# Kernel optimization log

Hardware: AMD Instinct MI355X
Metric: run time of the kernel (lower is better)

The kernel has to match this reference:

```python
import jax, jax.numpy as jnp
import numpy as np

B, S, D = 4, 4096, 256

def setup_inputs() -> dict:
    key = jax.random.key(0)
    ks = jax.random.split(key, 7)
    scale = 1.0 / np.sqrt(D)
    return {
        "x": jax.random.normal(ks[0], (B, S, D), dtype=jnp.float32),
        "Wq": jax.random.normal(ks[1], (D, D), dtype=jnp.float32) * scale,
        "bq": jnp.zeros((D,), dtype=jnp.float32),
        "Wk": jax.random.normal(ks[2], (D, D), dtype=jnp.float32) * scale,
        "bk": jnp.zeros((D,), dtype=jnp.float32),
        "Wv": jax.random.normal(ks[3], (D, D), dtype=jnp.float32) * scale,
        "bv": jnp.zeros((D,), dtype=jnp.float32),
    }

def reference(x, Wq, bq, Wk, bk, Wv, bv):
    # Dense projections (Keras Dense: x @ W + b)
    q = x @ Wq + bq  # [B,S,D]
    k = x @ Wk + bk
    v = x @ Wv + bv
    # Unscaled attention: softmax(Q K^T) V + residual
    scores = jnp.einsum("bsd,btd->bst", q, k)  # [B,S,S]
    attn = jax.nn.softmax(scores, axis=-1)
    out = jnp.einsum("bst,btd->bsd", attn, v)
    return out + x
```

## Files before the change

kernel.cpp:

```cpp
#include <hip/hip_runtime.h>
#include <stdint.h>

#define NB   4
#define SEQ  4096
#define DIM  256
#define NROW (NB*SEQ)

using bf16x8   = __attribute__((ext_vector_type(8))) __bf16;
using half8    = __attribute__((ext_vector_type(8))) _Float16;
using f32x4    = __attribute__((ext_vector_type(4))) float;
using f32x16   = __attribute__((ext_vector_type(16))) float;
using u32x4    = __attribute__((ext_vector_type(4))) unsigned int;
using ushort4t = __attribute__((ext_vector_type(4))) unsigned short;

__device__ __forceinline__ unsigned f2bf(float f){
    unsigned u = __builtin_bit_cast(unsigned, f);
    return (u + 0x7fffu + ((u >> 16) & 1u)) >> 16;
}
__device__ __forceinline__ float bf2f(unsigned b){
    return __builtin_bit_cast(float, b << 16);
}

#define MFMA(a,b,c)   __builtin_amdgcn_mfma_f32_16x16x32_bf16((a),(b),(c),0,0,0)
#define MFMAQK(a,b,c) __builtin_amdgcn_mfma_f32_32x32x16_f16((a),(b),(c),0,0,0)
#define MFMAPV(a,b,c) __builtin_amdgcn_mfma_f32_32x32x16_bf16((a),(b),(c),0,0,0)

__device__ __forceinline__ void gld16(const void* g, void* l){
    __builtin_amdgcn_global_load_lds(
        (const __attribute__((address_space(1))) void*)g,
        (__attribute__((address_space(3))) void*)l, 16, 0, 0);
}

__global__ __launch_bounds__(256) void convert_w_kernel(
    const float* __restrict__ Wq, const float* __restrict__ Wk,
    const float* __restrict__ Wv,
    unsigned short* __restrict__ WtHi, unsigned short* __restrict__ WtLo)
{
    int mat = blockIdx.y;
    const float* W = (mat == 0) ? Wq : (mat == 1 ? Wk : Wv);
    int id = blockIdx.x * 256 + threadIdx.x;
    int k = id >> 8, n = id & 255;
    float v = W[id];
    unsigned hi = f2bf(v);
    unsigned lo = f2bf(v - bf2f(hi));
    int nh = n >> 7, nt = (n >> 4) & 7, q16 = n & 15;
    int kc = k >> 5, g = (k >> 3) & 3, j = k & 7;
    int lane = g * 16 + q16;
    int o = ((((mat * 2 + nh) * 8 + nt) * 8 + kc) * 64 + lane) * 8 + j;
    WtHi[o] = (unsigned short)hi;
    WtLo[o] = (unsigned short)lo;
}

__global__ __launch_bounds__(256) void proj_kernel(
    const float* __restrict__ x,
    const unsigned short* __restrict__ WtHi, const unsigned short* __restrict__ WtLo,
    const float* __restrict__ bq, const float* __restrict__ bk,
    const float* __restrict__ bv,
    _Float16* __restrict__ Qf, _Float16* __restrict__ Kf,
    unsigned short* __restrict__ Vt)
{
    const int tid = threadIdx.x, lane = tid & 63, wid = tid >> 6;
    const int g = lane >> 4, q16 = lane & 15;
    const int mbase = blockIdx.x * 64 + wid * 16;
    const int nh = blockIdx.y;

    f32x4 acc[3][8];
    #pragma unroll
    for (int m = 0; m < 3; m++)
        #pragma unroll
        for (int n = 0; n < 8; n++) acc[m][n] = f32x4{0.f, 0.f, 0.f, 0.f};

    const float* xr = x + (mbase + q16) * DIM;

    for (int kc = 0; kc < 8; kc++) {
        const float* p = xr + kc * 32 + 8 * g;
        f32x4 va = *(const f32x4*)p;
        f32x4 vb = *(const f32x4*)(p + 4);
        float fv[8] = {va[0], va[1], va[2], va[3], vb[0], vb[1], vb[2], vb[3]};
        unsigned hw[4], lw[4];
        #pragma unroll
        for (int i = 0; i < 4; i++) {
            unsigned h0 = f2bf(fv[2*i]),              h1 = f2bf(fv[2*i+1]);
            unsigned l0 = f2bf(fv[2*i]   - bf2f(h0)), l1 = f2bf(fv[2*i+1] - bf2f(h1));
            hw[i] = h0 | (h1 << 16);
            lw[i] = l0 | (l1 << 16);
        }
        bf16x8 ahi = __builtin_bit_cast(bf16x8, u32x4{hw[0], hw[1], hw[2], hw[3]});
        bf16x8 alo = __builtin_bit_cast(bf16x8, u32x4{lw[0], lw[1], lw[2], lw[3]});

        #pragma unroll
        for (int mat = 0; mat < 3; mat++) {
            #pragma unroll
            for (int nt = 0; nt < 8; nt++) {
                const int fbase =
                    ((((mat * 2 + nh) * 8 + nt) * 8 + kc) * 64 + lane) * 8;
                bf16x8 bh = *(const bf16x8*)(WtHi + fbase);
                bf16x8 bl = *(const bf16x8*)(WtLo + fbase);
                acc[mat][nt] = MFMA(ahi, bh, acc[mat][nt]);
                acc[mat][nt] = MFMA(ahi, bl, acc[mat][nt]);
                acc[mat][nt] = MFMA(alo, bh, acc[mat][nt]);
            }
        }
    }

    #pragma unroll
    for (int nt = 0; nt < 8; nt++) {
        int ncol = nh * 128 + nt * 16 + q16;
        {
            float bb = bq[ncol];
            f32x4 c = acc[0][nt];
            #pragma unroll
            for (int r = 0; r < 4; r++)
                Qf[(size_t)(mbase + 4*g + r) * DIM + ncol] = (_Float16)(c[r] + bb);
        }
        {
            float bb = bk[ncol];
            f32x4 c = acc[1][nt];
            #pragma unroll
            for (int r = 0; r < 4; r++)
                Kf[(size_t)(mbase + 4*g + r) * DIM + ncol] = (_Float16)(c[r] + bb);
        }
        {
            float bb = bv[ncol];
            f32x4 c = acc[2][nt];
            ushort4t pk;
            #pragma unroll
            for (int r = 0; r < 4; r++) pk[r] = (unsigned short)f2bf(c[r] + bb);
            int m0 = mbase + 4 * g;
            int bat = m0 >> 12, s0 = m0 & 4095;
            *(ushort4t*)(Vt + (size_t)(bat * DIM + ncol) * SEQ + s0) = pk;
        }
    }
}

#define KLDS  0
#define VLDS  32768
#define BUFSZ 65536

__global__ __launch_bounds__(512, 1) void flash_kernel(
    const _Float16* __restrict__ Qf, const _Float16* __restrict__ Kf,
    const unsigned short* __restrict__ Vt,
    unsigned short* __restrict__ O0, unsigned short* __restrict__ O1,
    unsigned short* __restrict__ O2, unsigned short* __restrict__ O3,
    float2* __restrict__ ml0, float2* __restrict__ ml1,
    float2* __restrict__ ml2, float2* __restrict__ ml3)
{
    __shared__ __align__(16) unsigned char smem[131072];

    const int tid = threadIdx.x, lane = tid & 63, wid = tid >> 6;
    const int r32 = lane & 31, h = lane >> 5;
    const int qrow0 = blockIdx.x * 256;
    const int b = qrow0 >> 12;
    const int split = blockIdx.y;
    const int kvbase = split * 1024;
    const int stp = wid & 1;

    half8 qf[16];
    {
        const _Float16* qp = Qf + (size_t)(qrow0 + wid * 32 + r32) * DIM;
        #pragma unroll
        for (int s = 0; s < 16; s++)
            qf[s] = *(const half8*)(qp + s * 16 + h * 8);
    }

    f32x16 o[8];
    #pragma unroll
    for (int i = 0; i < 8; i++)
        #pragma unroll
        for (int j = 0; j < 16; j++) o[i][j] = 0.f;
    float m_run = -3.0e38f, l_run = 0.f;

    auto stage = [&](int chunk, int buf) {
        const int kv0 = kvbase + chunk * 64;
        unsigned char* base = smem + buf * BUFSZ;
        #pragma unroll
        for (int i = 0; i < 4; i++) {
            const int t = wid * 4 + i;
            const int krow = 2 * t + h;
            const int ksl  = (lane & 31) ^ (krow & 7);
            gld16(Kf + (size_t)(b * SEQ + kv0 + krow) * DIM + ksl * 8,
                  base + KLDS + t * 1024);
            const int d   = 8 * t + (lane >> 3);
            const int vsl = (lane & 7) ^ (d & 7);
            gld16(Vt + (size_t)(b * DIM + d) * SEQ + kv0 + vsl * 8,
                  base + VLDS + t * 1024);
        }
    };

    stage(0, 0);
    __syncthreads();

    for (int c = 0; c < 16; c++) {
        const int bf = c & 1;
        if (c + 1 < 16) stage(c + 1, bf ^ 1);

        const unsigned char* kb = smem + bf * BUFSZ;
        const unsigned char* vb = kb + VLDS;

        #pragma unroll
        for (int ii = 0; ii < 2; ii++) {
            const int st = ii ^ stp;
            f32x16 a;
            #pragma unroll
            for (int j = 0; j < 16; j++) a[j] = 0.f;
            __builtin_amdgcn_s_setprio(1);
            #pragma unroll
            for (int s = 0; s < 16; s++) {
                const int off = (st * 32 + r32) * 512
                              + (((2 * s + h) ^ (r32 & 7)) * 16);
                half8 kf = *(const half8*)(kb + KLDS + off);
                a = MFMAQK(kf, qf[s], a);
            }
            __builtin_amdgcn_s_setprio(0);

            float pm = a[0];
            #pragma unroll
            for (int j = 1; j < 16; j++) pm = fmaxf(pm, a[j]);
            pm = fmaxf(pm, __shfl_xor(pm, 32, 64));
            const bool defer = __all(pm <= m_run + 8.0f) != 0;
            const float mn = defer ? m_run : fmaxf(m_run, pm);
            const float sc = defer ? 1.0f : __expf(m_run - mn);
            float e[16]; float ps = 0.f;
            #pragma unroll
            for (int j = 0; j < 16; j++) { e[j] = __expf(a[j] - mn); ps += e[j]; }
            ps += __shfl_xor(ps, 32, 64);
            l_run = l_run * sc + ps;
            m_run = mn;

            unsigned w[8];
            #pragma unroll
            for (int t = 0; t < 8; t++)
                asm("v_cvt_pk_bf16_f32 %0, %1, %2"
                    : "=v"(w[t]) : "v"(e[2 * t]), "v"(e[2 * t + 1]));
            asm volatile("v_permlane32_swap_b32 %0, %1" : "+v"(w[0]), "+v"(w[2]));
            asm volatile("v_permlane32_swap_b32 %0, %1" : "+v"(w[1]), "+v"(w[3]));
            asm volatile("v_permlane32_swap_b32 %0, %1" : "+v"(w[4]), "+v"(w[6]));
            asm volatile("v_permlane32_swap_b32 %0, %1" : "+v"(w[5]), "+v"(w[7]));
            bf16x8 pA = __builtin_bit_cast(bf16x8, u32x4{w[0], w[1], w[2], w[3]});
            bf16x8 pB = __builtin_bit_cast(bf16x8, u32x4{w[4], w[5], w[6], w[7]});

            __builtin_amdgcn_s_setprio(1);
            #pragma unroll
            for (int dt = 0; dt < 8; dt++) {
                const int d = dt * 32 + r32;
                const int sw = d & 7;
                bf16x8 v0 = *(const bf16x8*)(vb + d * 128
                               + (((st * 4 + h)     ^ sw) * 16));
                bf16x8 v1 = *(const bf16x8*)(vb + d * 128
                               + (((st * 4 + 2 + h) ^ sw) * 16));
                f32x16 oo = o[dt];
                if (!defer) {
                    #pragma unroll
                    for (int j = 0; j < 16; j++) oo[j] *= sc;
                }
                oo = MFMAPV(v0, pA, oo);
                oo = MFMAPV(v1, pB, oo);
                o[dt] = oo;
            }
            __builtin_amdgcn_s_setprio(0);
        }

        __syncthreads();
    }

    if (h == 0) {
        float2* mlp = (split == 0) ? ml0 : (split == 1) ? ml1
                    : (split == 2) ? ml2 : ml3;
        mlp[qrow0 + wid * 32 + r32] = float2{m_run, l_run};
    }

    unsigned short* oP = (split == 0) ? O0 : (split == 1) ? O1
                       : (split == 2) ? O2 : O3;
    float* T = (float*)smem;
    #pragma unroll
    for (int dt = 0; dt < 8; dt++) {
        __syncthreads();
        #pragma unroll
        for (int j = 0; j < 16; j++) {
            const int dloc = (j & 3) + 8 * (j >> 2) + 4 * h;
            T[(wid * 32 + r32) * 33 + dloc] = o[dt][j];
        }
        __syncthreads();
        #pragma unroll
        for (int rq = 0; rq < 4; rq++) {
            const int q = wid * 32 + rq * 8 + (lane >> 3);
            const float* tr = T + q * 33 + (lane & 7) * 4;
            ushort4t pk;
            #pragma unroll
            for (int r = 0; r < 4; r++) pk[r] = (unsigned short)f2bf(tr[r]);
            *(ushort4t*)(oP + (size_t)(qrow0 + q) * DIM
                         + dt * 32 + (lane & 7) * 4) = pk;
        }
    }
}

__global__ __launch_bounds__(256) void combine_kernel(
    const unsigned short* __restrict__ o0, const unsigned short* __restrict__ o1,
    const unsigned short* __restrict__ o2, const unsigned short* __restrict__ o3,
    const float2* __restrict__ ml0, const float2* __restrict__ ml1,
    const float2* __restrict__ ml2, const float2* __restrict__ ml3,
    const float* __restrict__ x, float* __restrict__ out)
{
    int row = blockIdx.x * 4 + (threadIdx.x >> 6);
    int c0  = (threadIdx.x & 63) * 4;
    float2 A = ml0[row], B = ml1[row], C = ml2[row], D = ml3[row];
    float M  = fmaxf(fmaxf(A.x, B.x), fmaxf(C.x, D.x));
    float w0 = __expf(A.x - M), w1 = __expf(B.x - M);
    float w2 = __expf(C.x - M), w3 = __expf(D.x - M);
    float inv = 1.0f / (w0 * A.y + w1 * B.y + w2 * C.y + w3 * D.y);
    size_t base = (size_t)row * DIM + c0;
    ushort4t u0 = *(const ushort4t*)(o0 + base);
    ushort4t u1 = *(const ushort4t*)(o1 + base);
    ushort4t u2 = *(const ushort4t*)(o2 + base);
    ushort4t u3 = *(const ushort4t*)(o3 + base);
    f32x4    xr = *(const f32x4*)(x + base);
    f32x4 res;
    #pragma unroll
    for (int j = 0; j < 4; j++)
        res[j] = (w0 * bf2f((unsigned)u0[j]) + w1 * bf2f((unsigned)u1[j])
                + w2 * bf2f((unsigned)u2[j]) + w3 * bf2f((unsigned)u3[j])) * inv
                + xr[j];
    *(f32x4*)(out + base) = res;
}

extern "C" void kernel_launch(void* const* d_in, const int* in_sizes, int n_in,
                              void* d_out, int out_size, void* d_ws, size_t ws_size,
                              hipStream_t stream)
{
    const float* x  = (const float*)d_in[0];
    const float* Wq = (const float*)d_in[1];
    const float* bq = (const float*)d_in[2];
    const float* Wk = (const float*)d_in[3];
    const float* bk = (const float*)d_in[4];
    const float* Wv = (const float*)d_in[5];
    const float* bv = (const float*)d_in[6];
    float* out = (float*)d_out;

    unsigned char* ws = (unsigned char*)d_ws;
    _Float16*       Qf   = (_Float16*)(ws);
    _Float16*       Kf   = (_Float16*)(ws +  8388608);
    unsigned short* Vt   = (unsigned short*)(ws + 16777216);
    unsigned short* WtHi = (unsigned short*)(ws + 25165824);
    unsigned short* WtLo = (unsigned short*)(ws + 25559040);
    unsigned short* O0   = (unsigned short*)(ws + 25952256);
    unsigned short* O1   = (unsigned short*)(ws + 34340864);
    unsigned short* O2   = (unsigned short*)(ws + 42729472);
    unsigned short* O3   = (unsigned short*)(ws + 51118080);
    float2*         ML0  = (float2*)       (ws + 59506688);
    float2*         ML1  = (float2*)       (ws + 59637760);
    float2*         ML2  = (float2*)       (ws + 59768832);
    float2*         ML3  = (float2*)       (ws + 59899904);

    convert_w_kernel<<<dim3(256, 3), 256, 0, stream>>>(Wq, Wk, Wv, WtHi, WtLo);
    proj_kernel<<<dim3(256, 2), 256, 0, stream>>>(x, WtHi, WtLo, bq, bk, bv,
                                                  Qf, Kf, Vt);
    flash_kernel<<<dim3(64, 4), 512, 0, stream>>>(Qf, Kf, Vt,
                                                  O0, O1, O2, O3,
                                                  ML0, ML1, ML2, ML3);
    combine_kernel<<<4096, 256, 0, stream>>>(O0, O1, O2, O3,
                                             ML0, ML1, ML2, ML3, x, out);
}
```

Baseline: 181.1 us.

## Stage projection weights in LDS and split QK MFMA chain into two accumulators

```diff
diff --git a/kernel.cpp b/kernel.cpp
--- a/kernel.cpp
+++ b/kernel.cpp
@@ -59,6 +59,8 @@
     _Float16* __restrict__ Qf, _Float16* __restrict__ Kf,
     unsigned short* __restrict__ Vt)
 {
+    __shared__ __align__(16) unsigned char wsm[49152];
+
     const int tid = threadIdx.x, lane = tid & 63, wid = tid >> 6;
     const int g = lane >> 4, q16 = lane & 15;
     const int mbase = blockIdx.x * 64 + wid * 16;
@@ -73,6 +75,16 @@
     const float* xr = x + (mbase + q16) * DIM;
 
     for (int kc = 0; kc < 8; kc++) {
+        __syncthreads();
+        #pragma unroll
+        for (int i = 0; i < 12; i++) {
+            const int idx = wid * 12 + i;
+            const int mat = idx >> 4, nt = (idx >> 1) & 7, pl = idx & 1;
+            const size_t fb =
+                ((size_t)(((mat * 2 + nh) * 8 + nt) * 8 + kc)) * 512 + lane * 8;
+            gld16((pl ? WtLo : WtHi) + fb, wsm + idx * 1024);
+        }
+
         const float* p = xr + kc * 32 + 8 * g;
         f32x4 va = *(const f32x4*)p;
         f32x4 vb = *(const f32x4*)(p + 4);
@@ -88,14 +100,15 @@
         bf16x8 ahi = __builtin_bit_cast(bf16x8, u32x4{hw[0], hw[1], hw[2], hw[3]});
         bf16x8 alo = __builtin_bit_cast(bf16x8, u32x4{lw[0], lw[1], lw[2], lw[3]});
 
+        __syncthreads();
+
         #pragma unroll
         for (int mat = 0; mat < 3; mat++) {
             #pragma unroll
             for (int nt = 0; nt < 8; nt++) {
-                const int fbase =
-                    ((((mat * 2 + nh) * 8 + nt) * 8 + kc) * 64 + lane) * 8;
-                bf16x8 bh = *(const bf16x8*)(WtHi + fbase);
-                bf16x8 bl = *(const bf16x8*)(WtLo + fbase);
+                const int sidx = mat * 16 + nt * 2;
+                bf16x8 bh = *(const bf16x8*)(wsm + sidx * 1024 + lane * 16);
+                bf16x8 bl = *(const bf16x8*)(wsm + (sidx + 1) * 1024 + lane * 16);
                 acc[mat][nt] = MFMA(ahi, bh, acc[mat][nt]);
                 acc[mat][nt] = MFMA(ahi, bl, acc[mat][nt]);
                 acc[mat][nt] = MFMA(alo, bh, acc[mat][nt]);
@@ -200,18 +213,22 @@
         #pragma unroll
         for (int ii = 0; ii < 2; ii++) {
             const int st = ii ^ stp;
-            f32x16 a;
-            #pragma unroll
-            for (int j = 0; j < 16; j++) a[j] = 0.f;
+            f32x16 a0, a1;
+            #pragma unroll
+            for (int j = 0; j < 16; j++) { a0[j] = 0.f; a1[j] = 0.f; }
             __builtin_amdgcn_s_setprio(1);
             #pragma unroll
-            for (int s = 0; s < 16; s++) {
-                const int off = (st * 32 + r32) * 512
-                              + (((2 * s + h) ^ (r32 & 7)) * 16);
-                half8 kf = *(const half8*)(kb + KLDS + off);
-                a = MFMAQK(kf, qf[s], a);
+            for (int s = 0; s < 16; s += 2) {
+                const int rb = (st * 32 + r32) * 512;
+                const int off0 = rb + (((2 * s + h)     ^ (r32 & 7)) * 16);
+                const int off1 = rb + (((2 * s + 2 + h) ^ (r32 & 7)) * 16);
+                half8 kf0 = *(const half8*)(kb + KLDS + off0);
+                half8 kf1 = *(const half8*)(kb + KLDS + off1);
+                a0 = MFMAQK(kf0, qf[s],     a0);
+                a1 = MFMAQK(kf1, qf[s + 1], a1);
             }
             __builtin_amdgcn_s_setprio(0);
+            f32x16 a = a0 + a1;
 
             float pm = a[0];
             #pragma unroll
```

After: 189.1 us. 4.4% more time.
